# Kernel optimization log

Measured on AMD Instinct MI355X. Metric: run time of the kernel, lower is better.

## Reference

```python
import jax, jax.numpy as jnp
import numpy as np

N_NODES = 100000
N_EDGES = 3200000
N_GRAPHS = 64
NODE_FEATS = 32
LATENT = [32, 32, 32, 1]
OUT_DIM = 128
TOTAL_LATENT = sum(LATENT)  # 97


def setup_inputs() -> dict:
    key = jax.random.key(0)
    ks = jax.random.split(key, 16)
    node_feat = jax.random.normal(ks[0], (N_NODES, NODE_FEATS), dtype=jnp.float32)
    src = jax.random.randint(ks[1], (N_EDGES,), 0, N_NODES)
    dst = jax.random.randint(ks[2], (N_EDGES,), 0, N_NODES)
    graph_ids = jnp.sort(jax.random.randint(ks[3], (N_NODES,), 0, N_GRAPHS))
    # layer weights: Linear(in, out) -> W [in, out], b [out]
    dims = [NODE_FEATS] + LATENT
    inp = {
        'node_feat': node_feat,
        'src': src,
        'dst': dst,
        'graph_ids': graph_ids,
        'num_graphs': N_GRAPHS,
    }
    for i in range(len(LATENT)):
        inp[f'W{i}'] = 0.1 * jax.random.normal(ks[4 + 2 * i], (dims[i], dims[i + 1]), dtype=jnp.float32)
        inp[f'b{i}'] = 0.1 * jax.random.normal(ks[5 + 2 * i], (dims[i + 1],), dtype=jnp.float32)
    inp['Wout'] = 0.1 * jax.random.normal(ks[12], (TOTAL_LATENT, OUT_DIM), dtype=jnp.float32)
    inp['bout'] = 0.1 * jax.random.normal(ks[13], (OUT_DIM,), dtype=jnp.float32)
    return inp


def reference(node_feat, W0, b0, W1, b1, W2, b2, W3, b3, Wout, bout,
              src, dst, graph_ids, num_graphs):
    N = node_feat.shape[0]
    # node_degs = deg + 1 (adjacency row sums + 1)
    degs = jax.ops.segment_sum(jnp.ones_like(dst, dtype=node_feat.dtype), dst, num_segments=N)
    node_degs = (degs + 1.0)[:, None]  # [N, 1]

    params = [(W0, b0), (W1, b1), (W2, b2), (W3, b3)]
    h = node_feat
    cats = []
    for W, b in params:
        # n2npool = A @ h + h  (sparse SpMM via edge-list segment sum)
        agg = jax.ops.segment_sum(h[src], dst, num_segments=N) + h
        h = jnp.tanh((agg @ W + b) / node_degs)
        cats.append(h)
    hcat = jnp.concatenate(cats, axis=1)  # [N, 97]

    # per-graph sum pooling
    pooled = jax.ops.segment_sum(hcat, graph_ids, num_segments=num_graphs)  # [G, 97]
    # relu(relu(linear)) == relu(linear)
    out = jax.nn.relu(pooled @ Wout + bout)
    return out
```

## Files before the change

kernel.cpp:

```cpp
#include <hip/hip_runtime.h>
#include <hip/hip_bf16.h>


#define NFEAT 32
#define TOTLAT 97
#define NGRAPH 64
#define OUTDIM 128
#define BSHIFT 9
#define NPB 512
#define MAXBUCK 256
#define CH 8192

__global__ __launch_bounds__(256) void hist_kernel(const int* __restrict__ dst,
                                                   int* __restrict__ bucket_cnt,
                                                   int E, int nbuck) {
    __shared__ int h[MAXBUCK];
    for (int i = threadIdx.x; i < nbuck; i += blockDim.x) h[i] = 0;
    __syncthreads();
    int e0 = blockIdx.x * CH, e1 = min(e0 + CH, E);
    const int4* d4 = (const int4*)dst;
    int k0 = e0 >> 2, nk = (e1 - e0) >> 2;
    for (int k = k0 + threadIdx.x; k < k0 + nk; k += blockDim.x) {
        int4 v = d4[k];
        atomicAdd(&h[v.x >> BSHIFT], 1);
        atomicAdd(&h[v.y >> BSHIFT], 1);
        atomicAdd(&h[v.z >> BSHIFT], 1);
        atomicAdd(&h[v.w >> BSHIFT], 1);
    }
    for (int e = e0 + (nk << 2) + threadIdx.x; e < e1; e += blockDim.x)
        atomicAdd(&h[dst[e] >> BSHIFT], 1);
    __syncthreads();
    for (int i = threadIdx.x; i < nbuck; i += blockDim.x)
        if (h[i]) atomicAdd(&bucket_cnt[i], h[i]);
}

__global__ void bucket_scan_kernel(const int* __restrict__ bucket_cnt,
                                   int* __restrict__ bucket_start,
                                   int* __restrict__ bucket_cursor,
                                   int* __restrict__ row_ptr,
                                   int N, int E, int nbuck) {
    __shared__ int s[MAXBUCK];
    int i = threadIdx.x;
    int v = (i < nbuck) ? bucket_cnt[i] : 0;
    s[i] = v;
    __syncthreads();
    for (int d = 1; d < MAXBUCK; d <<= 1) {
        int t = (i >= d) ? s[i - d] : 0;
        __syncthreads();
        if (i >= d) s[i] += t;
        __syncthreads();
    }
    if (i < nbuck) {
        int excl = s[i] - v;
        bucket_start[i] = excl;
        bucket_cursor[i] = excl;
    }
    if (i == 0) { bucket_start[nbuck] = E; row_ptr[N] = E; }
}

__global__ __launch_bounds__(256) void part_kernel(const int* __restrict__ src,
                                                   const int* __restrict__ dst,
                                                   int* __restrict__ bucket_cursor,
                                                   int2* __restrict__ pairs,
                                                   int E, int nbuck) {
    __shared__ int h[MAXBUCK];
    __shared__ int gb[MAXBUCK];
    for (int i = threadIdx.x; i < nbuck; i += blockDim.x) h[i] = 0;
    __syncthreads();
    int e0 = blockIdx.x * CH, e1 = min(e0 + CH, E);
    const int4* d4 = (const int4*)dst;
    const int4* s4 = (const int4*)src;
    int k0 = e0 >> 2, nk = (e1 - e0) >> 2;
    for (int k = k0 + threadIdx.x; k < k0 + nk; k += blockDim.x) {
        int4 v = d4[k];
        atomicAdd(&h[v.x >> BSHIFT], 1);
        atomicAdd(&h[v.y >> BSHIFT], 1);
        atomicAdd(&h[v.z >> BSHIFT], 1);
        atomicAdd(&h[v.w >> BSHIFT], 1);
    }
    for (int e = e0 + (nk << 2) + threadIdx.x; e < e1; e += blockDim.x)
        atomicAdd(&h[dst[e] >> BSHIFT], 1);
    __syncthreads();
    for (int i = threadIdx.x; i < nbuck; i += blockDim.x) {
        int c = h[i];
        gb[i] = c ? atomicAdd(&bucket_cursor[i], c) : 0;
        h[i] = 0;
    }
    __syncthreads();
    for (int k = k0 + threadIdx.x; k < k0 + nk; k += blockDim.x) {
        int4 d = d4[k];
        int4 s = s4[k];
        int b, r;
        b = d.x >> BSHIFT; r = atomicAdd(&h[b], 1); pairs[gb[b] + r] = make_int2(s.x, d.x);
        b = d.y >> BSHIFT; r = atomicAdd(&h[b], 1); pairs[gb[b] + r] = make_int2(s.y, d.y);
        b = d.z >> BSHIFT; r = atomicAdd(&h[b], 1); pairs[gb[b] + r] = make_int2(s.z, d.z);
        b = d.w >> BSHIFT; r = atomicAdd(&h[b], 1); pairs[gb[b] + r] = make_int2(s.w, d.w);
    }
    for (int e = e0 + (nk << 2) + threadIdx.x; e < e1; e += blockDim.x) {
        int dv = dst[e];
        int b = dv >> BSHIFT;
        int r = atomicAdd(&h[b], 1);
        pairs[gb[b] + r] = make_int2(src[e], dv);
    }
}

__global__ __launch_bounds__(NPB) void csr_kernel(const int2* __restrict__ pairs,
                                                  const int* __restrict__ bucket_start,
                                                  int* __restrict__ row_ptr,
                                                  int* __restrict__ col_idx,
                                                  float* __restrict__ inv_deg, int N) {
    __shared__ int deg[NPB];
    __shared__ int scn[NPB];
    int b = blockIdx.x;
    int n0 = b << BSHIFT;
    int tid = threadIdx.x;
    deg[tid] = 0;
    __syncthreads();
    int e0 = bucket_start[b], e1 = bucket_start[b + 1];
    for (int e = e0 + tid; e < e1; e += NPB) {
        int2 p = pairs[e];
        atomicAdd(&deg[p.y - n0], 1);
    }
    __syncthreads();
    int v = deg[tid];
    scn[tid] = v;
    __syncthreads();
    for (int d = 1; d < NPB; d <<= 1) {
        int t = (tid >= d) ? scn[tid - d] : 0;
        __syncthreads();
        if (tid >= d) scn[tid] += t;
        __syncthreads();
    }
    int excl = scn[tid] - v;
    int n = n0 + tid;
    if (n < N) {
        row_ptr[n] = e0 + excl;
        inv_deg[n] = 1.0f / ((float)v + 1.0f);
    }
    deg[tid] = excl;
    __syncthreads();
    for (int e = e0 + tid; e < e1; e += NPB) {
        int2 p = pairs[e];
        int r = atomicAdd(&deg[p.y - n0], 1);
        col_idx[e0 + r] = p.x;
    }
}

__global__ __launch_bounds__(256, 8) void agg_kernel(
    const float* __restrict__ h_in, float* __restrict__ agg,
    const int* __restrict__ row_ptr, const int* __restrict__ col_idx, int N)
{
    const int t = blockIdx.x * blockDim.x + threadIdx.x;
    int n = t >> 3;
    const int l8 = t & 7;
    if (n >= N) return;

    const float4* __restrict__ h4 = (const float4*)h_in;

    int beg = row_ptr[n];
    int end = row_ptr[n + 1];
    int len = end - beg;
    float4 self = h4[(size_t)n * 8 + l8];
    float4 acc = self;

    for (int e = beg; e < end; e += 32) {
        int base = e + l8 * 4;
        int my0 = __builtin_nontemporal_load(&col_idx[base + 0]);
        int my1 = __builtin_nontemporal_load(&col_idx[base + 1]);
        int my2 = __builtin_nontemporal_load(&col_idx[base + 2]);
        int my3 = __builtin_nontemporal_load(&col_idx[base + 3]);
        int rem = end - e;
#pragma unroll
        for (int sl = 0; sl < 8; ++sl) {
            int i0 = __shfl(my0, sl, 8);
            int i1 = __shfl(my1, sl, 8);
            int i2 = __shfl(my2, sl, 8);
            int i3 = __shfl(my3, sl, 8);
            int j = sl * 4;
            i0 = (j + 0 < rem) ? i0 : n;
            i1 = (j + 1 < rem) ? i1 : n;
            i2 = (j + 2 < rem) ? i2 : n;
            i3 = (j + 3 < rem) ? i3 : n;
            float4 v0 = h4[(size_t)i0 * 8 + l8];
            float4 v1 = h4[(size_t)i1 * 8 + l8];
            float4 v2 = h4[(size_t)i2 * 8 + l8];
            float4 v3 = h4[(size_t)i3 * 8 + l8];
            acc.x += v0.x + v1.x + v2.x + v3.x;
            acc.y += v0.y + v1.y + v2.y + v3.y;
            acc.z += v0.z + v1.z + v2.z + v3.z;
            acc.w += v0.w + v1.w + v2.w + v3.w;
        }
    }
    float fk = (float)(((len + 31) & ~31) - len);
    acc.x -= fk * self.x; acc.y -= fk * self.y;
    acc.z -= fk * self.z; acc.w -= fk * self.w;

    ((float4*)agg)[(size_t)n * 8 + l8] = acc;
}

template <bool EMIT_Y>
__global__ __launch_bounds__(256) void mlp_kernel(
    float* __restrict__ hbuf,
    const float* __restrict__ W, const float* __restrict__ b,
    const float* __restrict__ inv_deg, const int* __restrict__ graph_ids,
    float* __restrict__ pooled, int pool_col,
    const float* __restrict__ W3, float* __restrict__ y, int N)
{
    const int t = blockIdx.x * blockDim.x + threadIdx.x;
    int n = t >> 3;
    const int l8 = t & 7;
    const int f0 = l8 * 4;
    const int lane = threadIdx.x & 63;
    const bool valid = n < N;
    if (!valid) n = N - 1;

    float4 acc = ((const float4*)hbuf)[(size_t)n * 8 + l8];
    float ideg = inv_deg[n];
    int g = graph_ids[n];
    int g0 = __builtin_amdgcn_readfirstlane(g);
    bool g_uniform = __all(g == g0);

    float4 o = *(const float4*)&b[f0];
#pragma unroll
    for (int sl = 0; sl < 8; ++sl) {
        float a0 = __shfl(acc.x, sl, 8);
        float a1 = __shfl(acc.y, sl, 8);
        float a2 = __shfl(acc.z, sl, 8);
        float a3 = __shfl(acc.w, sl, 8);
        float4 w0 = *(const float4*)&W[(sl * 4 + 0) * NFEAT + f0];
        float4 w1 = *(const float4*)&W[(sl * 4 + 1) * NFEAT + f0];
        float4 w2 = *(const float4*)&W[(sl * 4 + 2) * NFEAT + f0];
        float4 w3 = *(const float4*)&W[(sl * 4 + 3) * NFEAT + f0];
        o.x += a0 * w0.x + a1 * w1.x + a2 * w2.x + a3 * w3.x;
        o.y += a0 * w0.y + a1 * w1.y + a2 * w2.y + a3 * w3.y;
        o.z += a0 * w0.z + a1 * w1.z + a2 * w2.z + a3 * w3.z;
        o.w += a0 * w0.w + a1 * w1.w + a2 * w2.w + a3 * w3.w;
    }
    float4 v;
    v.x = tanhf(o.x * ideg);
    v.y = tanhf(o.y * ideg);
    v.z = tanhf(o.z * ideg);
    v.w = tanhf(o.w * ideg);

    if (!EMIT_Y) {
        if (valid)
            ((float4*)hbuf)[(size_t)n * 8 + l8] = v;
    } else {
        float4 wv = *(const float4*)&W3[f0];
        float p = v.x * wv.x + v.y * wv.y + v.z * wv.z + v.w * wv.w;
        p += __shfl_xor(p, 1);
        p += __shfl_xor(p, 2);
        p += __shfl_xor(p, 4);
        if (valid && l8 == 0) y[n] = p;
    }

    float4 c;
    c.x = valid ? v.x : 0.0f;
    c.y = valid ? v.y : 0.0f;
    c.z = valid ? v.z : 0.0f;
    c.w = valid ? v.w : 0.0f;
    if (g_uniform) {
        c.x += __shfl_xor(c.x, 8);  c.x += __shfl_xor(c.x, 16);  c.x += __shfl_xor(c.x, 32);
        c.y += __shfl_xor(c.y, 8);  c.y += __shfl_xor(c.y, 16);  c.y += __shfl_xor(c.y, 32);
        c.z += __shfl_xor(c.z, 8);  c.z += __shfl_xor(c.z, 16);  c.z += __shfl_xor(c.z, 32);
        c.w += __shfl_xor(c.w, 8);  c.w += __shfl_xor(c.w, 16);  c.w += __shfl_xor(c.w, 32);
        if (lane < 8) {
            float* p = &pooled[g0 * TOTLAT + pool_col + f0];
            atomicAdd(p + 0, c.x);
            atomicAdd(p + 1, c.y);
            atomicAdd(p + 2, c.z);
            atomicAdd(p + 3, c.w);
        }
    } else if (valid) {
        float* p = &pooled[g * TOTLAT + pool_col + f0];
        atomicAdd(p + 0, v.x);
        atomicAdd(p + 1, v.y);
        atomicAdd(p + 2, v.z);
        atomicAdd(p + 3, v.w);
    }
}

__global__ __launch_bounds__(256) void agg3_kernel(
    const float* __restrict__ y, const float* __restrict__ b3,
    const int* __restrict__ row_ptr, const int* __restrict__ col_idx,
    const float* __restrict__ inv_deg, const int* __restrict__ graph_ids,
    float* __restrict__ pooled, int N)
{
    int n = blockIdx.x * blockDim.x + threadIdx.x;
    const bool valid = n < N;
    if (!valid) n = N - 1;

    int beg = row_ptr[n];
    int end = row_ptr[n + 1];
    float s = y[n];
    int e = beg;
    for (; e + 8 <= end; e += 8) {
        float a0 = y[col_idx[e + 0]];
        float a1 = y[col_idx[e + 1]];
        float a2 = y[col_idx[e + 2]];
        float a3 = y[col_idx[e + 3]];
        float a4 = y[col_idx[e + 4]];
        float a5 = y[col_idx[e + 5]];
        float a6 = y[col_idx[e + 6]];
        float a7 = y[col_idx[e + 7]];
        s += ((a0 + a1) + (a2 + a3)) + ((a4 + a5) + (a6 + a7));
    }
    for (; e < end; ++e)
        s += y[col_idx[e]];

    float v = tanhf((s + b3[0]) * inv_deg[n]);

    int g = graph_ids[n];
    int g0 = __builtin_amdgcn_readfirstlane(g);
    float c = valid ? v : 0.0f;
    if (__all(g == g0)) {
        c += __shfl_xor(c, 1);  c += __shfl_xor(c, 2);  c += __shfl_xor(c, 4);
        c += __shfl_xor(c, 8);  c += __shfl_xor(c, 16); c += __shfl_xor(c, 32);
        if ((threadIdx.x & 63) == 0)
            atomicAdd(&pooled[g0 * TOTLAT + 96], c);
    } else if (valid) {
        atomicAdd(&pooled[g * TOTLAT + 96], v);
    }
}

__global__ void final_kernel(const float* __restrict__ pooled, const float* __restrict__ Wout,
                             const float* __restrict__ bout, float* __restrict__ out) {
    int g = blockIdx.x;
    int o = threadIdx.x;
    float s = bout[o];
#pragma unroll 4
    for (int k = 0; k < TOTLAT; ++k)
        s += pooled[g * TOTLAT + k] * Wout[k * OUTDIM + o];
    out[g * OUTDIM + o] = fmaxf(s, 0.0f);
}

extern "C" void kernel_launch(void* const* d_in, const int* in_sizes, int n_in,
                              void* d_out, int out_size, void* d_ws, size_t ws_size,
                              hipStream_t stream) {
    const float* node_feat = (const float*)d_in[0];
    const int*   src       = (const int*)d_in[1];
    const int*   dst       = (const int*)d_in[2];
    const int*   graph_ids = (const int*)d_in[3];
    const float* W0 = (const float*)d_in[5];
    const float* b0 = (const float*)d_in[6];
    const float* W1 = (const float*)d_in[7];
    const float* b1 = (const float*)d_in[8];
    const float* W2 = (const float*)d_in[9];
    const float* b2 = (const float*)d_in[10];
    const float* W3 = (const float*)d_in[11];
    const float* b3 = (const float*)d_in[12];
    const float* Wout = (const float*)d_in[13];
    const float* bout = (const float*)d_in[14];
    float* out = (float*)d_out;

    const int N = in_sizes[0] / NFEAT;
    const int E = in_sizes[1];
    const int nbuck = (N + NPB - 1) >> BSHIFT;

    char* ws = (char*)d_ws;
    size_t off = 0;
    auto carve = [&](size_t bytes) -> void* {
        void* p = ws + off;
        off = (off + bytes + 255) & ~(size_t)255;
        return p;
    };
    int*   bucket_cnt    = (int*)carve((size_t)MAXBUCK * 4);
    int*   bucket_start  = (int*)carve((size_t)(MAXBUCK + 1) * 4);
    int*   bucket_cursor = (int*)carve((size_t)MAXBUCK * 4);
    int*   row_ptr       = (int*)carve((size_t)(N + 1) * 4);
    int*   col_idx       = (int*)carve((size_t)(E + 32) * 4);
    float* inv_deg       = (float*)carve((size_t)N * 4);
    float* hA            = (float*)carve((size_t)N * NFEAT * 4);
    float* hB            = (float*)carve((size_t)N * NFEAT * 4);
    float* y             = (float*)carve((size_t)N * 4);
    float* pooled        = (float*)carve((size_t)NGRAPH * TOTLAT * 4);
    int2*  pairs         = (int2*)hA;

    hipMemsetAsync(bucket_cnt, 0, (size_t)MAXBUCK * 4, stream);
    hipMemsetAsync(pooled, 0, (size_t)NGRAPH * TOTLAT * 4, stream);

    const int nchunks = (E + CH - 1) / CH;
    hist_kernel<<<nchunks, 256, 0, stream>>>(dst, bucket_cnt, E, nbuck);
    bucket_scan_kernel<<<1, MAXBUCK, 0, stream>>>(bucket_cnt, bucket_start, bucket_cursor,
                                                  row_ptr, N, E, nbuck);
    part_kernel<<<nchunks, 256, 0, stream>>>(src, dst, bucket_cursor, pairs, E, nbuck);
    csr_kernel<<<nbuck, NPB, 0, stream>>>(pairs, bucket_start, row_ptr, col_idx, inv_deg, N);

    const int lblocks = (N * 8 + 255) / 256;
    agg_kernel<<<lblocks, 256, 0, stream>>>(node_feat, hA, row_ptr, col_idx, N);
    mlp_kernel<false><<<lblocks, 256, 0, stream>>>(hA, W0, b0, inv_deg, graph_ids,
                                                   pooled, 0, nullptr, nullptr, N);
    agg_kernel<<<lblocks, 256, 0, stream>>>(hA, hB, row_ptr, col_idx, N);
    mlp_kernel<false><<<lblocks, 256, 0, stream>>>(hB, W1, b1, inv_deg, graph_ids,
                                                   pooled, 32, nullptr, nullptr, N);
    agg_kernel<<<lblocks, 256, 0, stream>>>(hB, hA, row_ptr, col_idx, N);
    mlp_kernel<true><<<lblocks, 256, 0, stream>>>(hA, W2, b2, inv_deg, graph_ids,
                                                  pooled, 64, W3, y, N);
    agg3_kernel<<<(N + 255) / 256, 256, 0, stream>>>(y, b3, row_ptr, col_idx, inv_deg,
                                                     graph_ids, pooled, N);

    final_kernel<<<NGRAPH, OUTDIM, 0, stream>>>(pooled, Wout, bout, out);
}
```

Baseline: 584.6 us.

## Fuse aggregation with MLP per layer and defer graph pooling to separate kernel

Merges each neighbor-aggregation kernel with its dense layer so the aggregated features go through shared memory instead of a global round trip, and removes one launch per layer. Pooling is moved out of the per-layer kernels into a dedicated kernel that binary-searches the sorted graph_ids and reduces per graph segment, which needs a third hidden buffer and a z buffer. tanhf is replaced with an exp-based approximation. The trade-off is extra workspace, one more full read of all hidden states for pooling, and slightly different numerics from the fast tanh.

```diff
diff --git a/kernel.cpp b/kernel.cpp
--- a/kernel.cpp
+++ b/kernel.cpp
@@ -10,6 +10,12 @@
 #define NPB 512
 #define MAXBUCK 256
 #define CH 8192
+
+__device__ __forceinline__ float ftanh(float x) {
+    x = fminf(fmaxf(x, -15.0f), 15.0f);
+    float t = __expf(2.0f * x);
+    return (t - 1.0f) / (t + 1.0f);
+}
 
 __global__ __launch_bounds__(256) void hist_kernel(const int* __restrict__ dst,
                                                    int* __restrict__ bucket_cnt,
@@ -146,14 +152,20 @@
     }
 }
 
-__global__ __launch_bounds__(256, 8) void agg_kernel(
-    const float* __restrict__ h_in, float* __restrict__ agg,
-    const int* __restrict__ row_ptr, const int* __restrict__ col_idx, int N)
+template <bool WRITE_Y>
+__global__ __launch_bounds__(256, 8) void layer_fused(
+    const float* __restrict__ h_in, float* __restrict__ h_out,
+    const float* __restrict__ W, const float* __restrict__ bvec,
+    const int* __restrict__ row_ptr, const int* __restrict__ col_idx,
+    const float* __restrict__ inv_deg,
+    const float* __restrict__ W3, float* __restrict__ y, int N)
 {
+    __shared__ float accs[32][33];
     const int t = blockIdx.x * blockDim.x + threadIdx.x;
     int n = t >> 3;
     const int l8 = t & 7;
-    if (n >= N) return;
+    const bool valid = n < N;
+    if (!valid) n = N - 1;
 
     const float4* __restrict__ h4 = (const float4*)h_in;
 
@@ -195,100 +207,47 @@
     acc.x -= fk * self.x; acc.y -= fk * self.y;
     acc.z -= fk * self.z; acc.w -= fk * self.w;
 
-    ((float4*)agg)[(size_t)n * 8 + l8] = acc;
-}
-
-template <bool EMIT_Y>
-__global__ __launch_bounds__(256) void mlp_kernel(
-    float* __restrict__ hbuf,
-    const float* __restrict__ W, const float* __restrict__ b,
-    const float* __restrict__ inv_deg, const int* __restrict__ graph_ids,
-    float* __restrict__ pooled, int pool_col,
-    const float* __restrict__ W3, float* __restrict__ y, int N)
-{
-    const int t = blockIdx.x * blockDim.x + threadIdx.x;
-    int n = t >> 3;
-    const int l8 = t & 7;
+    const int gl = threadIdx.x >> 3;
     const int f0 = l8 * 4;
-    const int lane = threadIdx.x & 63;
-    const bool valid = n < N;
-    if (!valid) n = N - 1;
-
-    float4 acc = ((const float4*)hbuf)[(size_t)n * 8 + l8];
+    accs[gl][f0 + 0] = acc.x;
+    accs[gl][f0 + 1] = acc.y;
+    accs[gl][f0 + 2] = acc.z;
+    accs[gl][f0 + 3] = acc.w;
+
+    float4 o = *(const float4*)&bvec[f0];
+#pragma unroll 8
+    for (int k = 0; k < NFEAT; ++k) {
+        float a = accs[gl][k];
+        float4 w = *(const float4*)&W[k * NFEAT + f0];
+        o.x += a * w.x; o.y += a * w.y; o.z += a * w.z; o.w += a * w.w;
+    }
     float ideg = inv_deg[n];
-    int g = graph_ids[n];
-    int g0 = __builtin_amdgcn_readfirstlane(g);
-    bool g_uniform = __all(g == g0);
-
-    float4 o = *(const float4*)&b[f0];
-#pragma unroll
-    for (int sl = 0; sl < 8; ++sl) {
-        float a0 = __shfl(acc.x, sl, 8);
-        float a1 = __shfl(acc.y, sl, 8);
-        float a2 = __shfl(acc.z, sl, 8);
-        float a3 = __shfl(acc.w, sl, 8);
-        float4 w0 = *(const float4*)&W[(sl * 4 + 0) * NFEAT + f0];
-        float4 w1 = *(const float4*)&W[(sl * 4 + 1) * NFEAT + f0];
-        float4 w2 = *(const float4*)&W[(sl * 4 + 2) * NFEAT + f0];
-        float4 w3 = *(const float4*)&W[(sl * 4 + 3) * NFEAT + f0];
-        o.x += a0 * w0.x + a1 * w1.x + a2 * w2.x + a3 * w3.x;
-        o.y += a0 * w0.y + a1 * w1.y + a2 * w2.y + a3 * w3.y;
-        o.z += a0 * w0.z + a1 * w1.z + a2 * w2.z + a3 * w3.z;
-        o.w += a0 * w0.w + a1 * w1.w + a2 * w2.w + a3 * w3.w;
-    }
     float4 v;
-    v.x = tanhf(o.x * ideg);
-    v.y = tanhf(o.y * ideg);
-    v.z = tanhf(o.z * ideg);
-    v.w = tanhf(o.w * ideg);
-
-    if (!EMIT_Y) {
-        if (valid)
-            ((float4*)hbuf)[(size_t)n * 8 + l8] = v;
-    } else {
-        float4 wv = *(const float4*)&W3[f0];
-        float p = v.x * wv.x + v.y * wv.y + v.z * wv.z + v.w * wv.w;
-        p += __shfl_xor(p, 1);
-        p += __shfl_xor(p, 2);
-        p += __shfl_xor(p, 4);
-        if (valid && l8 == 0) y[n] = p;
-    }
-
-    float4 c;
-    c.x = valid ? v.x : 0.0f;
-    c.y = valid ? v.y : 0.0f;
-    c.z = valid ? v.z : 0.0f;
-    c.w = valid ? v.w : 0.0f;
-    if (g_uniform) {
-        c.x += __shfl_xor(c.x, 8);  c.x += __shfl_xor(c.x, 16);  c.x += __shfl_xor(c.x, 32);
-        c.y += __shfl_xor(c.y, 8);  c.y += __shfl_xor(c.y, 16);  c.y += __shfl_xor(c.y, 32);
-        c.z += __shfl_xor(c.z, 8);  c.z += __shfl_xor(c.z, 16);  c.z += __shfl_xor(c.z, 32);
-        c.w += __shfl_xor(c.w, 8);  c.w += __shfl_xor(c.w, 16);  c.w += __shfl_xor(c.w, 32);
-        if (lane < 8) {
-            float* p = &pooled[g0 * TOTLAT + pool_col + f0];
-            atomicAdd(p + 0, c.x);
-            atomicAdd(p + 1, c.y);
-            atomicAdd(p + 2, c.z);
-            atomicAdd(p + 3, c.w);
+    v.x = ftanh(o.x * ideg);
+    v.y = ftanh(o.y * ideg);
+    v.z = ftanh(o.z * ideg);
+    v.w = ftanh(o.w * ideg);
+
+    if (valid) {
+        *(float4*)&h_out[(size_t)n * NFEAT + f0] = v;
+        if (WRITE_Y) {
+            float4 wv = *(const float4*)&W3[f0];
+            float p = v.x * wv.x + v.y * wv.y + v.z * wv.z + v.w * wv.w;
+            p += __shfl_xor(p, 1);
+            p += __shfl_xor(p, 2);
+            p += __shfl_xor(p, 4);
+            if (l8 == 0) y[n] = p;
         }
-    } else if (valid) {
-        float* p = &pooled[g * TOTLAT + pool_col + f0];
-        atomicAdd(p + 0, v.x);
-        atomicAdd(p + 1, v.y);
-        atomicAdd(p + 2, v.z);
-        atomicAdd(p + 3, v.w);
     }
 }
 
 __global__ __launch_bounds__(256) void agg3_kernel(
     const float* __restrict__ y, const float* __restrict__ b3,
     const int* __restrict__ row_ptr, const int* __restrict__ col_idx,
-    const float* __restrict__ inv_deg, const int* __restrict__ graph_ids,
-    float* __restrict__ pooled, int N)
+    const float* __restrict__ inv_deg, float* __restrict__ z, int N)
 {
     int n = blockIdx.x * blockDim.x + threadIdx.x;
-    const bool valid = n < N;
-    if (!valid) n = N - 1;
+    if (n >= N) return;
 
     int beg = row_ptr[n];
     int end = row_ptr[n + 1];
@@ -308,19 +267,50 @@
     for (; e < end; ++e)
         s += y[col_idx[e]];
 
-    float v = tanhf((s + b3[0]) * inv_deg[n]);
-
-    int g = graph_ids[n];
-    int g0 = __builtin_amdgcn_readfirstlane(g);
-    float c = valid ? v : 0.0f;
-    if (__all(g == g0)) {
-        c += __shfl_xor(c, 1);  c += __shfl_xor(c, 2);  c += __shfl_xor(c, 4);
-        c += __shfl_xor(c, 8);  c += __shfl_xor(c, 16); c += __shfl_xor(c, 32);
-        if ((threadIdx.x & 63) == 0)
-            atomicAdd(&pooled[g0 * TOTLAT + 96], c);
-    } else if (valid) {
-        atomicAdd(&pooled[g * TOTLAT + 96], v);
-    }
+    z[n] = ftanh((s + b3[0]) * inv_deg[n]);
+}
+
+__global__ __launch_bounds__(128) void pool_kernel(
+    const float* __restrict__ h0, const float* __restrict__ h1,
+    const float* __restrict__ h2, const float* __restrict__ z,
+    const int* __restrict__ graph_ids, float* __restrict__ pooled, int N)
+{
+    __shared__ int sb[2];
+    int g = blockIdx.x >> 2, q = blockIdx.x & 3;
+    if (threadIdx.x == 0) {
+        int lo = 0, hi = N;
+        while (lo < hi) { int m = (lo + hi) >> 1; if (graph_ids[m] < g) lo = m + 1; else hi = m; }
+        sb[0] = lo;
+        lo = 0; hi = N;
+        while (lo < hi) { int m = (lo + hi) >> 1; if (graph_ids[m] < g + 1) lo = m + 1; else hi = m; }
+        sb[1] = lo;
+    }
+    __syncthreads();
+    int s = sb[0], e = sb[1];
+    int per = (e - s + 3) >> 2;
+    int ns = s + q * per;
+    int ne = min(ns + per, e);
+    int c = threadIdx.x;
+    if (c >= TOTLAT || ns >= ne) return;
+
+    float sum = 0.0f;
+    if (c < 32) {
+        const float* p = h0 + c;
+#pragma unroll 4
+        for (int n = ns; n < ne; ++n) sum += p[(size_t)n * NFEAT];
+    } else if (c < 64) {
+        const float* p = h1 + (c - 32);
+#pragma unroll 4
+        for (int n = ns; n < ne; ++n) sum += p[(size_t)n * NFEAT];
+    } else if (c < 96) {
+        const float* p = h2 + (c - 64);
+#pragma unroll 4
+        for (int n = ns; n < ne; ++n) sum += p[(size_t)n * NFEAT];
+    } else {
+#pragma unroll 4
+        for (int n = ns; n < ne; ++n) sum += z[n];
+    }
+    atomicAdd(&pooled[g * TOTLAT + c], sum);
 }
 
 __global__ void final_kernel(const float* __restrict__ pooled, const float* __restrict__ Wout,
@@ -372,7 +362,9 @@
     float* inv_deg       = (float*)carve((size_t)N * 4);
     float* hA            = (float*)carve((size_t)N * NFEAT * 4);
     float* hB            = (float*)carve((size_t)N * NFEAT * 4);
+    float* hC            = (float*)carve((size_t)N * NFEAT * 4);
     float* y             = (float*)carve((size_t)N * 4);
+    float* z             = (float*)carve((size_t)N * 4);
     float* pooled        = (float*)carve((size_t)NGRAPH * TOTLAT * 4);
     int2*  pairs         = (int2*)hA;
 
@@ -387,17 +379,14 @@
     csr_kernel<<<nbuck, NPB, 0, stream>>>(pairs, bucket_start, row_ptr, col_idx, inv_deg, N);
 
     const int lblocks = (N * 8 + 255) / 256;
-    agg_kernel<<<lblocks, 256, 0, stream>>>(node_feat, hA, row_ptr, col_idx, N);
-    mlp_kernel<false><<<lblocks, 256, 0, stream>>>(hA, W0, b0, inv_deg, graph_ids,
-                                                   pooled, 0, nullptr, nullptr, N);
-    agg_kernel<<<lblocks, 256, 0, stream>>>(hA, hB, row_ptr, col_idx, N);
-    mlp_kernel<false><<<lblocks, 256, 0, stream>>>(hB, W1, b1, inv_deg, graph_ids,
-                                                   pooled, 32, nullptr, nullptr, N);
-    agg_kernel<<<lblocks, 256, 0, stream>>>(hB, hA, row_ptr, col_idx, N);
-    mlp_kernel<true><<<lblocks, 256, 0, stream>>>(hA, W2, b2, inv_deg, graph_ids,
-                                                  pooled, 64, W3, y, N);
-    agg3_kernel<<<(N + 255) / 256, 256, 0, stream>>>(y, b3, row_ptr, col_idx, inv_deg,
-                                                     graph_ids, pooled, N);
-
+    layer_fused<false><<<lblocks, 256, 0, stream>>>(node_feat, hA, W0, b0, row_ptr, col_idx,
+                                                    inv_deg, nullptr, nullptr, N);
+    layer_fused<false><<<lblocks, 256, 0, stream>>>(hA, hB, W1, b1, row_ptr, col_idx,
+                                                    inv_deg, nullptr, nullptr, N);
+    layer_fused<true><<<lblocks, 256, 0, stream>>>(hB, hC, W2, b2, row_ptr, col_idx,
+                                                   inv_deg, W3, y, N);
+    agg3_kernel<<<(N + 255) / 256, 256, 0, stream>>>(y, b3, row_ptr, col_idx, inv_deg, z, N);
+
+    pool_kernel<<<NGRAPH * 4, 128, 0, stream>>>(hA, hB, hC, z, graph_ids, pooled, N);
     final_kernel<<<NGRAPH, OUTDIM, 0, stream>>>(pooled, Wout, bout, out);
 }
```

Result: faster. 520.5 us (-11.0%).
